# Kernel tuning notes

Measured on AMD Instinct MI355X. Metric: run time of the kernel, lower is better.

Reference implementation:

```python
import jax, jax.numpy as jnp
import numpy as np

B, S, D = 2, 2048, 2048
H, HKV, HD = 16, 4, 128
GROUPS = H // HKV
SCALE = HD ** -0.5
ROPE_THETA = 10000.0
NEG = -1e9


def _rope_cos_sin():
    inv_freq = 1.0 / (ROPE_THETA ** (jnp.arange(0, HD, 2, dtype=jnp.float32) / HD))  # [HD/2]
    pos = jnp.arange(S, dtype=jnp.float32)
    freqs = pos[:, None] * inv_freq[None, :]            # [S, HD/2]
    emb = jnp.concatenate([freqs, freqs], axis=-1)      # [S, HD]
    cos = jnp.broadcast_to(jnp.cos(emb)[None], (B, S, HD))
    sin = jnp.broadcast_to(jnp.sin(emb)[None], (B, S, HD))
    return cos, sin


def setup_inputs() -> dict:
    key = jax.random.key(0)
    ks = jax.random.split(key, 5)
    hidden_states = jax.random.normal(ks[0], (B, S, D), dtype=jnp.float32)
    cos, sin = _rope_cos_sin()
    causal = jnp.where(jnp.arange(S)[:, None] >= jnp.arange(S)[None, :], 0.0, NEG).astype(jnp.float32)
    attn_mask = jnp.broadcast_to(causal[None, None], (B, 1, S, S))
    wq = jax.random.normal(ks[1], (H * HD, D), dtype=jnp.float32) * (D ** -0.5)
    wk = jax.random.normal(ks[2], (HKV * HD, D), dtype=jnp.float32) * (D ** -0.5)
    wv = jax.random.normal(ks[3], (HKV * HD, D), dtype=jnp.float32) * (D ** -0.5)
    wo = jax.random.normal(ks[4], (D, H * HD), dtype=jnp.float32) * (D ** -0.5)
    return {"hidden_states": hidden_states, "cos": cos, "sin": sin,
            "attn_mask": attn_mask, "wq": wq, "wk": wk, "wv": wv, "wo": wo}


def _rotate_half(x):
    x1, x2 = x[..., : HD // 2], x[..., HD // 2:]
    return jnp.concatenate([-x2, x1], axis=-1)


def reference(hidden_states, cos, sin, attn_mask, wq, wk, wv, wo):
    # projections (torch Linear: x @ W.T), reshape to [B, heads, S, HD]
    q = (hidden_states @ wq.T).reshape(B, S, H, HD).transpose(0, 2, 1, 3)
    k = (hidden_states @ wk.T).reshape(B, S, HKV, HD).transpose(0, 2, 1, 3)
    v = (hidden_states @ wv.T).reshape(B, S, HKV, HD).transpose(0, 2, 1, 3)
    # RoPE (cos/sin broadcast over head dim)
    c = cos[:, None, :, :]
    s = sin[:, None, :, :]
    q = q * c + _rotate_half(q) * s
    k = k * c + _rotate_half(k) * s
    # GQA: repeat each kv head GROUPS times consecutively (matches repeat_kv)
    k = jnp.repeat(k, GROUPS, axis=1)
    v = jnp.repeat(v, GROUPS, axis=1)
    logits = jnp.einsum('bhqd,bhkd->bhqk', q, k) * SCALE + attn_mask
    w = jax.nn.softmax(logits.astype(jnp.float32), axis=-1).astype(q.dtype)
    out = jnp.einsum('bhqk,bhkd->bhqd', w, v)            # [B,H,S,HD]
    out = out.transpose(0, 2, 1, 3).reshape(B, S, H * HD)
    return out @ wo.T
```

## Files before the change

kernel.cpp:

```cpp
#include <hip/hip_runtime.h>

typedef __attribute__((ext_vector_type(8))) short bf16x8;
typedef __attribute__((ext_vector_type(4))) float f32x4;
typedef __attribute__((ext_vector_type(8))) unsigned short u16x8;
typedef unsigned short u16;

#define GLOBAL_AS __attribute__((address_space(1)))
#define LDS_AS __attribute__((address_space(3)))

#define S_ 2048
#define SCALE_ 0.08838834764831845f

static __device__ __forceinline__ u16 f2bf(float f) {
  unsigned u = __builtin_bit_cast(unsigned, f);
  u += 0x7fffu + ((u >> 16) & 1u);
  return (u16)(u >> 16);
}
static __device__ __forceinline__ float bf2f(u16 h) {
  return __builtin_bit_cast(float, ((unsigned)h) << 16);
}

__global__ __launch_bounds__(256) void cvt_bf16(const float* __restrict__ src,
                                                u16* __restrict__ dst, long n) {
  long i = ((long)blockIdx.x * 256 + threadIdx.x) * 8;
  if (i >= n) return;
  f32x4 a = *(const f32x4*)(src + i);
  f32x4 b = *(const f32x4*)(src + i + 4);
  u16x8 o;
  o[0] = f2bf(a[0]); o[1] = f2bf(a[1]); o[2] = f2bf(a[2]); o[3] = f2bf(a[3]);
  o[4] = f2bf(b[0]); o[5] = f2bf(b[1]); o[6] = f2bf(b[2]); o[7] = f2bf(b[3]);
  *(u16x8*)(dst + i) = o;
}

template <bool BF16OUT>
__global__ __launch_bounds__(256)
void gemm_bt(const u16* __restrict__ A, const u16* __restrict__ Bw,
             void* __restrict__ Cp, int M, int N, int K) {
  __shared__ u16 As[128 * 64];
  __shared__ u16 Bs[128 * 64];
  const int tid = threadIdx.x;
  const int wave = tid >> 6, lane = tid & 63;
  const int fr = lane & 15, fg = lane >> 4;
  const int wm = (wave >> 1) * 64, wn = (wave & 1) * 64;
  const long rowA = (long)blockIdx.y * 128;
  const long rowB = (long)blockIdx.x * 128;

  f32x4 acc[4][4] = {};

  for (int k0 = 0; k0 < K; k0 += 64) {
    __syncthreads();
#pragma unroll
    for (int c = 0; c < 4; ++c) {
      const int base = (wave * 4 + c) * 1024;
      const int off = base + lane * 16;
      const int r = off >> 7;
      const int kc = (off & 127) >> 1;
      __builtin_amdgcn_global_load_lds(
          (GLOBAL_AS void*)(A + (rowA + r) * (long)K + k0 + kc),
          (LDS_AS void*)(As + (base >> 1)), 16, 0, 0);
      __builtin_amdgcn_global_load_lds(
          (GLOBAL_AS void*)(Bw + (rowB + r) * (long)K + k0 + kc),
          (LDS_AS void*)(Bs + (base >> 1)), 16, 0, 0);
    }
    __syncthreads();
#pragma unroll
    for (int ks = 0; ks < 2; ++ks) {
      bf16x8 af[4], bfr[4];
#pragma unroll
      for (int i = 0; i < 4; ++i) {
        af[i]  = *(const bf16x8*)&As[(wm + i * 16 + fr) * 64 + ks * 32 + fg * 8];
        bfr[i] = *(const bf16x8*)&Bs[(wn + i * 16 + fr) * 64 + ks * 32 + fg * 8];
      }
#pragma unroll
      for (int i = 0; i < 4; ++i)
#pragma unroll
        for (int j = 0; j < 4; ++j)
          acc[i][j] = __builtin_amdgcn_mfma_f32_16x16x32_bf16(af[i], bfr[j], acc[i][j], 0, 0, 0);
    }
  }
#pragma unroll
  for (int i = 0; i < 4; ++i)
#pragma unroll
    for (int j = 0; j < 4; ++j)
#pragma unroll
      for (int r = 0; r < 4; ++r) {
        const long row = rowA + wm + i * 16 + fg * 4 + r;
        const long col = rowB + wn + j * 16 + fr;
        if (BF16OUT) ((u16*)Cp)[row * N + col] = f2bf(acc[i][j][r]);
        else         ((float*)Cp)[row * N + col] = acc[i][j][r];
      }
}

__global__ __launch_bounds__(256)
void rope_rearrange(const u16* __restrict__ QKV, const float* __restrict__ cosb,
                    const float* __restrict__ sinb, u16* __restrict__ Qr,
                    u16* __restrict__ Kr) {
  const int m = blockIdx.x;
  const int b = m >> 11, s = m & 2047;
  const int t = threadIdx.x;
  const u16* row = QKV + (long)m * 3072;
  const float* cp = cosb + (long)m * 128;
  const float* sp = sinb + (long)m * 128;
#pragma unroll
  for (int i = 0; i < 4; ++i) {
    const int idx = i * 256 + t;
    const int h = idx >> 6, d = idx & 63;
    const float x1 = bf2f(row[h * 128 + d]);
    const float x2 = bf2f(row[h * 128 + d + 64]);
    const float c = cp[d], sv = sp[d];
    const long o = ((long)(b * 16 + h) * S_ + s) * 128 + d;
    Qr[o] = f2bf(x1 * c - x2 * sv);
    Qr[o + 64] = f2bf(x2 * c + x1 * sv);
  }
  {
    const int h = t >> 6, d = t & 63;
    const float x1 = bf2f(row[2048 + h * 128 + d]);
    const float x2 = bf2f(row[2048 + h * 128 + d + 64]);
    const float c = cp[d], sv = sp[d];
    const long o = ((long)(b * 4 + h) * S_ + s) * 128 + d;
    Kr[o] = f2bf(x1 * c - x2 * sv);
    Kr[o + 64] = f2bf(x2 * c + x1 * sv);
  }
}

__global__ __launch_bounds__(256)
void transpose_v(const u16* __restrict__ QKV, u16* __restrict__ Vt) {
  __shared__ u16 t[32][33];
  const int s0 = blockIdx.x * 32, d0 = blockIdx.y * 32;
  const int bk = blockIdx.z;
  const int b = bk >> 2, kh = bk & 3;
  const int tx = threadIdx.x & 31, ty = threadIdx.x >> 5;
  const u16* src = QKV + 2560 + (long)kh * 128;
#pragma unroll
  for (int i = 0; i < 4; ++i) {
    const int sl = ty + i * 8;
    t[sl][tx] = src[(long)(b * S_ + s0 + sl) * 3072 + d0 + tx];
  }
  __syncthreads();
  u16* dst = Vt + (long)(b * 4 + kh) * 128 * S_;
#pragma unroll
  for (int i = 0; i < 4; ++i) {
    const int dl = ty + i * 8;
    dst[(long)(d0 + dl) * S_ + s0 + tx] = t[tx][dl];
  }
}

#define KVBLK 64
__global__ __launch_bounds__(256)
void attn_fwd(const u16* __restrict__ Qr, const u16* __restrict__ Kr,
              const u16* __restrict__ Vt, u16* __restrict__ Att) {
  __shared__ u16 Ks[KVBLK * 128];
  __shared__ u16 Vs[128 * KVBLK];
  __shared__ u16 Ps[4][16 * KVBLK];

  const int bh = blockIdx.y;
  const int b = bh >> 4, h = bh & 15;
  const int kh = h >> 2;
  const int tid = threadIdx.x, wave = tid >> 6, lane = tid & 63;
  const int fr = lane & 15, fg = lane >> 4;
  const int f7 = fr & 7;

  const u16* Qb = Qr + (long)(b * 16 + h) * S_ * 128;
  const u16* Kb = Kr + (long)(b * 4 + kh) * S_ * 128;
  const u16* Vg = Vt + (long)(b * 4 + kh) * 128 * (long)S_;
  u16* Pw = Ps[wave];

  for (int half = 0; half < 2; ++half) {
    const int qt = half ? (31 - blockIdx.x) : blockIdx.x;
    const int q0 = qt * 64;
    const int qbase = q0 + wave * 16;

    bf16x8 qf[4];
#pragma unroll
    for (int ks = 0; ks < 4; ++ks)
      qf[ks] = *(const bf16x8*)&Qb[(long)(qbase + fr) * 128 + ks * 32 + fg * 8];

    f32x4 acc[8] = {};
    float m_run[4], l_run[4];
#pragma unroll
    for (int r = 0; r < 4; ++r) { m_run[r] = -1e30f; l_run[r] = 0.f; }

    const int ntiles = qt + 1;
    for (int t = 0; t < ntiles; ++t) {
      const int kv0 = t * KVBLK;
      __syncthreads();
#pragma unroll
      for (int c = 0; c < 4; ++c) {
        const int slab = wave * 4 + c;
        const int offu = slab * 512 + lane * 8;
        const int kvl = offu >> 7;
        const int kc = ((offu >> 3) & 15) ^ (kvl & 7);
        __builtin_amdgcn_global_load_lds(
            (GLOBAL_AS void*)(Kb + (long)(kv0 + kvl) * 128 + kc * 8),
            (LDS_AS void*)(Ks + slab * 512), 16, 0, 0);
        const int dr = offu >> 6;
        const int vc = ((offu >> 3) & 7) ^ (dr & 7);
        __builtin_amdgcn_global_load_lds(
            (GLOBAL_AS void*)(Vg + (long)dr * S_ + kv0 + vc * 8),
            (LDS_AS void*)(Vs + slab * 512), 16, 0, 0);
      }
      __syncthreads();

      f32x4 sf[4] = {};
#pragma unroll
      for (int ks = 0; ks < 4; ++ks) {
        bf16x8 kf[4];
#pragma unroll
        for (int ni = 0; ni < 4; ++ni)
          kf[ni] = *(const bf16x8*)&Ks[(ni * 16 + fr) * 128 + (((ks * 4 + fg) ^ f7) << 3)];
        __builtin_amdgcn_s_setprio(1);
#pragma unroll
        for (int ni = 0; ni < 4; ++ni)
          sf[ni] = __builtin_amdgcn_mfma_f32_16x16x32_bf16(qf[ks], kf[ni], sf[ni], 0, 0, 0);
        __builtin_amdgcn_s_setprio(0);
      }

      float pr[4][4];
      float mx[4];
#pragma unroll
      for (int r = 0; r < 4; ++r) mx[r] = -3.0e38f;
#pragma unroll
      for (int ni = 0; ni < 4; ++ni) {
        const int kvg = kv0 + ni * 16 + fr;
#pragma unroll
        for (int r = 0; r < 4; ++r) {
          const int qrow = qbase + fg * 4 + r;
          float v = sf[ni][r] * SCALE_;
          if (kvg > qrow) v = -1e30f;
          pr[ni][r] = v;
          mx[r] = fmaxf(mx[r], v);
        }
      }
#pragma unroll
      for (int r = 0; r < 4; ++r) {
        mx[r] = fmaxf(mx[r], __shfl_xor(mx[r], 1));
        mx[r] = fmaxf(mx[r], __shfl_xor(mx[r], 2));
        mx[r] = fmaxf(mx[r], __shfl_xor(mx[r], 4));
        mx[r] = fmaxf(mx[r], __shfl_xor(mx[r], 8));
      }
      bool need = false;
#pragma unroll
      for (int r = 0; r < 4; ++r) need = need || (mx[r] > m_run[r] + 8.0f);
      if (__any(need)) {
#pragma unroll
        for (int r = 0; r < 4; ++r) {
          const float mn = fmaxf(m_run[r], mx[r]);
          const float scq = __expf(m_run[r] - mn);
          l_run[r] *= scq;
          m_run[r] = mn;
#pragma unroll
          for (int nj = 0; nj < 8; ++nj) acc[nj][r] *= scq;
        }
      }
      float rs[4] = {0.f, 0.f, 0.f, 0.f};
#pragma unroll
      for (int ni = 0; ni < 4; ++ni) {
        const int col = ni * 16 + fr;
        const int chs = col >> 3, wi = col & 7;
#pragma unroll
        for (int r = 0; r < 4; ++r) {
          const float e = __expf(pr[ni][r] - m_run[r]);
          rs[r] += e;
          const int row = fg * 4 + r;
          Pw[row * 64 + (((chs ^ (row & 7)) << 3) | wi)] = f2bf(e);
        }
      }
#pragma unroll
      for (int r = 0; r < 4; ++r) {
        rs[r] += __shfl_xor(rs[r], 1);
        rs[r] += __shfl_xor(rs[r], 2);
        rs[r] += __shfl_xor(rs[r], 4);
        rs[r] += __shfl_xor(rs[r], 8);
        l_run[r] += rs[r];
      }

      bf16x8 pf[2];
#pragma unroll
      for (int ks2 = 0; ks2 < 2; ++ks2)
        pf[ks2] = *(const bf16x8*)&Pw[fr * 64 + (((ks2 * 4 + fg) ^ f7) << 3)];
      __builtin_amdgcn_s_setprio(1);
#pragma unroll
      for (int nj = 0; nj < 8; ++nj) {
#pragma unroll
        for (int ks2 = 0; ks2 < 2; ++ks2) {
          const bf16x8 vf = *(const bf16x8*)&Vs[(nj * 16 + fr) * 64 + (((ks2 * 4 + fg) ^ f7) << 3)];
          acc[nj] = __builtin_amdgcn_mfma_f32_16x16x32_bf16(pf[ks2], vf, acc[nj], 0, 0, 0);
        }
      }
      __builtin_amdgcn_s_setprio(0);
    }

#pragma unroll
    for (int r = 0; r < 4; ++r) {
      const float inv = 1.0f / l_run[r];
      const long orow = ((long)b * S_ + qbase + fg * 4 + r) * 2048 + h * 128;
#pragma unroll
      for (int nj = 0; nj < 8; ++nj)
        Att[orow + nj * 16 + fr] = f2bf(acc[nj][r] * inv);
    }
  }
}

extern "C" void kernel_launch(void* const* d_in, const int* in_sizes, int n_in,
                              void* d_out, int out_size, void* d_ws, size_t ws_size,
                              hipStream_t stream) {
  const float* hidden = (const float*)d_in[0];
  const float* cosb = (const float*)d_in[1];
  const float* sinb = (const float*)d_in[2];
  const float* wq = (const float*)d_in[4];
  const float* wk = (const float*)d_in[5];
  const float* wv = (const float*)d_in[6];
  const float* wo = (const float*)d_in[7];
  float* out = (float*)d_out;

  u16* Xbf  = (u16*)d_ws;
  u16* Wqkv = Xbf + 8388608;
  u16* Wo   = Wqkv + 6291456;
  u16* QKV  = Wo + 4194304;
  u16* Qr   = QKV + 12582912;
  u16* Kr   = Qr + 8388608;
  u16* Vtp  = Kr + 2097152;
  u16* Att  = Xbf;
  if (ws_size < (size_t)44040192 * 2) return;

  cvt_bf16<<<dim3(4096), dim3(256), 0, stream>>>(hidden, Xbf, (long)8388608);
  cvt_bf16<<<dim3(2048), dim3(256), 0, stream>>>(wq, Wqkv, (long)4194304);
  cvt_bf16<<<dim3(512),  dim3(256), 0, stream>>>(wk, Wqkv + 4194304, (long)1048576);
  cvt_bf16<<<dim3(512),  dim3(256), 0, stream>>>(wv, Wqkv + 5242880, (long)1048576);
  cvt_bf16<<<dim3(2048), dim3(256), 0, stream>>>(wo, Wo, (long)4194304);

  gemm_bt<true><<<dim3(24, 32), dim3(256), 0, stream>>>(Xbf, Wqkv, (void*)QKV, 4096, 3072, 2048);
  rope_rearrange<<<dim3(4096), dim3(256), 0, stream>>>(QKV, cosb, sinb, Qr, Kr);
  transpose_v<<<dim3(64, 4, 8), dim3(256), 0, stream>>>(QKV, Vtp);
  attn_fwd<<<dim3(16, 32), dim3(256), 0, stream>>>(Qr, Kr, Vtp, Att);
  gemm_bt<false><<<dim3(16, 32), dim3(256), 0, stream>>>(Att, Wo, (void*)out, 4096, 2048, 2048);
}
```

Before: 268.0 us.

## Rewrite attention with 32x32 MFMA, register-resident P, and merged conversion launch

The attention kernel moves to 32x32x16 MFMAs with 128-row query tiles, computing S transposed so P stays in registers (packed via cvt_pk_bf16 and permlane32_swap) instead of going through LDS. Softmax scale and log2(e) are folded into K during RoPE so raw v_exp_f32 can be used. The five conversion launches are merged into one kernel. Trade-offs: more registers per lane, and causal imbalance because each block handles a single q tile with no pairing; waves whose rows are fully masked still take part in the loads and only skip compute.

```diff
diff --git a/kernel.cpp b/kernel.cpp
--- a/kernel.cpp
+++ b/kernel.cpp
@@ -2,7 +2,9 @@
 
 typedef __attribute__((ext_vector_type(8))) short bf16x8;
 typedef __attribute__((ext_vector_type(4))) float f32x4;
+typedef __attribute__((ext_vector_type(16))) float f32x16;
 typedef __attribute__((ext_vector_type(8))) unsigned short u16x8;
+typedef __attribute__((ext_vector_type(4))) unsigned u32x4;
 typedef unsigned short u16;
 
 #define GLOBAL_AS __attribute__((address_space(1)))
@@ -10,6 +12,7 @@
 
 #define S_ 2048
 #define SCALE_ 0.08838834764831845f
+#define SMK_ 0.12751741406106783f
 
 static __device__ __forceinline__ u16 f2bf(float f) {
   unsigned u = __builtin_bit_cast(unsigned, f);
@@ -19,11 +22,26 @@
 static __device__ __forceinline__ float bf2f(u16 h) {
   return __builtin_bit_cast(float, ((unsigned)h) << 16);
 }
-
-__global__ __launch_bounds__(256) void cvt_bf16(const float* __restrict__ src,
-                                                u16* __restrict__ dst, long n) {
-  long i = ((long)blockIdx.x * 256 + threadIdx.x) * 8;
-  if (i >= n) return;
+static __device__ __forceinline__ float exp2_raw(float x) {
+  float r; asm("v_exp_f32 %0, %1" : "=v"(r) : "v"(x)); return r;
+}
+static __device__ __forceinline__ unsigned cvtpk(float lo, float hi_) {
+  unsigned r; asm("v_cvt_pk_bf16_f32 %0, %1, %2" : "=v"(r) : "v"(lo), "v"(hi_)); return r;
+}
+
+__global__ __launch_bounds__(256)
+void cvt_all(const float* __restrict__ h, const float* __restrict__ wq,
+             const float* __restrict__ wk, const float* __restrict__ wv,
+             const float* __restrict__ wo, u16* __restrict__ Xbf,
+             u16* __restrict__ Wqkv, u16* __restrict__ Wo) {
+  const int bid = blockIdx.x;
+  const float* src; u16* dst; long base;
+  if (bid < 4096)      { src = h;  dst = Xbf;            base = (long)bid * 2048; }
+  else if (bid < 6144) { src = wq; dst = Wqkv;           base = (long)(bid - 4096) * 2048; }
+  else if (bid < 6656) { src = wk; dst = Wqkv + 4194304; base = (long)(bid - 6144) * 2048; }
+  else if (bid < 7168) { src = wv; dst = Wqkv + 5242880; base = (long)(bid - 6656) * 2048; }
+  else                 { src = wo; dst = Wo;             base = (long)(bid - 7168) * 2048; }
+  const long i = base + (long)threadIdx.x * 8;
   f32x4 a = *(const f32x4*)(src + i);
   f32x4 b = *(const f32x4*)(src + i + 4);
   u16x8 o;
@@ -118,8 +136,8 @@
     const float x2 = bf2f(row[2048 + h * 128 + d + 64]);
     const float c = cp[d], sv = sp[d];
     const long o = ((long)(b * 4 + h) * S_ + s) * 128 + d;
-    Kr[o] = f2bf(x1 * c - x2 * sv);
-    Kr[o + 64] = f2bf(x2 * c + x1 * sv);
+    Kr[o] = f2bf((x1 * c - x2 * sv) * SMK_);
+    Kr[o + 64] = f2bf((x2 * c + x1 * sv) * SMK_);
   }
 }
 
@@ -145,159 +163,151 @@
   }
 }
 
-#define KVBLK 64
+struct PA2 { bf16x8 a, b; };
+static __device__ __forceinline__ PA2 pack_half(const f32x16 s) {
+  PA2 out;
+#pragma unroll
+  for (int ks2 = 0; ks2 < 2; ++ks2) {
+    const int rb = ks2 * 8;
+    unsigned w0 = cvtpk(s[rb + 0], s[rb + 1]);
+    unsigned w1 = cvtpk(s[rb + 2], s[rb + 3]);
+    unsigned w2 = cvtpk(s[rb + 4], s[rb + 5]);
+    unsigned w3 = cvtpk(s[rb + 6], s[rb + 7]);
+    asm("v_permlane32_swap_b32 %0, %1" : "+v"(w0), "+v"(w2));
+    asm("v_permlane32_swap_b32 %0, %1" : "+v"(w1), "+v"(w3));
+    u32x4 pw; pw[0] = w0; pw[1] = w1; pw[2] = w2; pw[3] = w3;
+    if (ks2 == 0) out.a = __builtin_bit_cast(bf16x8, pw);
+    else          out.b = __builtin_bit_cast(bf16x8, pw);
+  }
+  return out;
+}
+
 __global__ __launch_bounds__(256)
 void attn_fwd(const u16* __restrict__ Qr, const u16* __restrict__ Kr,
               const u16* __restrict__ Vt, u16* __restrict__ Att) {
-  __shared__ u16 Ks[KVBLK * 128];
-  __shared__ u16 Vs[128 * KVBLK];
-  __shared__ u16 Ps[4][16 * KVBLK];
+  __shared__ u16 Ks[64 * 128];
+  __shared__ u16 Vs[128 * 64];
 
   const int bh = blockIdx.y;
   const int b = bh >> 4, h = bh & 15;
   const int kh = h >> 2;
+  const int qt = 15 - blockIdx.x;
+  const int q0 = qt * 128;
   const int tid = threadIdx.x, wave = tid >> 6, lane = tid & 63;
-  const int fr = lane & 15, fg = lane >> 4;
-  const int f7 = fr & 7;
+  const int l31 = lane & 31, hi = lane >> 5, r7 = lane & 7;
+  const int qwmin = q0 + wave * 32;
 
   const u16* Qb = Qr + (long)(b * 16 + h) * S_ * 128;
   const u16* Kb = Kr + (long)(b * 4 + kh) * S_ * 128;
   const u16* Vg = Vt + (long)(b * 4 + kh) * 128 * (long)S_;
-  u16* Pw = Ps[wave];
-
-  for (int half = 0; half < 2; ++half) {
-    const int qt = half ? (31 - blockIdx.x) : blockIdx.x;
-    const int q0 = qt * 64;
-    const int qbase = q0 + wave * 16;
-
-    bf16x8 qf[4];
-#pragma unroll
-    for (int ks = 0; ks < 4; ++ks)
-      qf[ks] = *(const bf16x8*)&Qb[(long)(qbase + fr) * 128 + ks * 32 + fg * 8];
-
-    f32x4 acc[8] = {};
-    float m_run[4], l_run[4];
-#pragma unroll
-    for (int r = 0; r < 4; ++r) { m_run[r] = -1e30f; l_run[r] = 0.f; }
-
-    const int ntiles = qt + 1;
-    for (int t = 0; t < ntiles; ++t) {
-      const int kv0 = t * KVBLK;
-      __syncthreads();
-#pragma unroll
-      for (int c = 0; c < 4; ++c) {
-        const int slab = wave * 4 + c;
-        const int offu = slab * 512 + lane * 8;
-        const int kvl = offu >> 7;
-        const int kc = ((offu >> 3) & 15) ^ (kvl & 7);
-        __builtin_amdgcn_global_load_lds(
-            (GLOBAL_AS void*)(Kb + (long)(kv0 + kvl) * 128 + kc * 8),
-            (LDS_AS void*)(Ks + slab * 512), 16, 0, 0);
-        const int dr = offu >> 6;
-        const int vc = ((offu >> 3) & 7) ^ (dr & 7);
-        __builtin_amdgcn_global_load_lds(
-            (GLOBAL_AS void*)(Vg + (long)dr * S_ + kv0 + vc * 8),
-            (LDS_AS void*)(Vs + slab * 512), 16, 0, 0);
-      }
-      __syncthreads();
-
-      f32x4 sf[4] = {};
+
+  bf16x8 qf[8];
+  const u16* qrow = Qb + (long)(qwmin + l31) * 128 + hi * 8;
+#pragma unroll
+  for (int ds = 0; ds < 8; ++ds) qf[ds] = *(const bf16x8*)(qrow + ds * 16);
+
+  f32x16 acc[4] = {};
+  float m_run = -1e30f, l_run = 0.f;
+  const int qg = qwmin + l31;
+
+  const int ntiles = 2 * (qt + 1);
+  for (int t = 0; t < ntiles; ++t) {
+    const int kv0 = t * 64;
+    __syncthreads();
+#pragma unroll
+    for (int c = 0; c < 4; ++c) {
+      const int slab = wave * 4 + c;
+      const int offu = slab * 512 + lane * 8;
+      const int kvl = offu >> 7;
+      const int kc = ((offu >> 3) & 15) ^ (kvl & 7);
+      __builtin_amdgcn_global_load_lds(
+          (GLOBAL_AS void*)(Kb + (long)(kv0 + kvl) * 128 + kc * 8),
+          (LDS_AS void*)(Ks + slab * 512), 16, 0, 0);
+      const int dr = offu >> 6;
+      const int vc = ((offu >> 3) & 7) ^ (dr & 7);
+      __builtin_amdgcn_global_load_lds(
+          (GLOBAL_AS void*)(Vg + (long)dr * S_ + kv0 + vc * 8),
+          (LDS_AS void*)(Vs + slab * 512), 16, 0, 0);
+    }
+    __syncthreads();
+
+    if (kv0 > qwmin + 31) continue;
+
+    f32x16 s0 = {}, s1 = {};
+    __builtin_amdgcn_s_setprio(1);
+#pragma unroll
+    for (int ds = 0; ds < 8; ++ds) {
+      const int ch = ((2 * ds + hi) ^ r7) << 3;
+      const bf16x8 ka0 = *(const bf16x8*)&Ks[l31 * 128 + ch];
+      const bf16x8 ka1 = *(const bf16x8*)&Ks[(32 + l31) * 128 + ch];
+      s0 = __builtin_amdgcn_mfma_f32_32x32x16_bf16(ka0, qf[ds], s0, 0, 0, 0);
+      s1 = __builtin_amdgcn_mfma_f32_32x32x16_bf16(ka1, qf[ds], s1, 0, 0, 0);
+    }
+    __builtin_amdgcn_s_setprio(0);
+
+    if (kv0 + 63 > qwmin) {
+#pragma unroll
+      for (int r = 0; r < 16; ++r) {
+        const int cr = (r & 3) + 8 * (r >> 2) + 4 * hi;
+        if (kv0 + cr > qg)      s0[r] = -3.0e38f;
+        if (kv0 + 32 + cr > qg) s1[r] = -3.0e38f;
+      }
+    }
+
+    float mx = s0[0];
+#pragma unroll
+    for (int r = 1; r < 16; ++r) mx = fmaxf(mx, s0[r]);
+#pragma unroll
+    for (int r = 0; r < 16; ++r) mx = fmaxf(mx, s1[r]);
+    mx = fmaxf(mx, __shfl_xor(mx, 32));
+
+    if (__any(mx > m_run + 8.0f)) {
+      const float mn = fmaxf(m_run, mx);
+      const float scq = exp2_raw(m_run - mn);
+      m_run = mn; l_run *= scq;
+#pragma unroll
+      for (int r = 0; r < 16; ++r) {
+        const int cr = (r & 3) + 8 * (r >> 2) + 4 * hi;
+        const float sr = __shfl(scq, cr);
+        acc[0][r] *= sr; acc[1][r] *= sr; acc[2][r] *= sr; acc[3][r] *= sr;
+      }
+    }
+
+    float rs = 0.f;
+#pragma unroll
+    for (int r = 0; r < 16; ++r) { s0[r] = exp2_raw(s0[r] - m_run); rs += s0[r]; }
+#pragma unroll
+    for (int r = 0; r < 16; ++r) { s1[r] = exp2_raw(s1[r] - m_run); rs += s1[r]; }
+    rs += __shfl_xor(rs, 32);
+    l_run += rs;
+
+    bf16x8 pa[4];
+    { PA2 p0 = pack_half(s0); pa[0] = p0.a; pa[1] = p0.b; }
+    { PA2 p1 = pack_half(s1); pa[2] = p1.a; pa[3] = p1.b; }
+
+    __builtin_amdgcn_s_setprio(1);
+#pragma unroll
+    for (int nj = 0; nj < 4; ++nj) {
+      const int vrow = (nj * 32 + l31) * 64;
 #pragma unroll
       for (int ks = 0; ks < 4; ++ks) {
-        bf16x8 kf[4];
-#pragma unroll
-        for (int ni = 0; ni < 4; ++ni)
-          kf[ni] = *(const bf16x8*)&Ks[(ni * 16 + fr) * 128 + (((ks * 4 + fg) ^ f7) << 3)];
-        __builtin_amdgcn_s_setprio(1);
-#pragma unroll
-        for (int ni = 0; ni < 4; ++ni)
-          sf[ni] = __builtin_amdgcn_mfma_f32_16x16x32_bf16(qf[ks], kf[ni], sf[ni], 0, 0, 0);
-        __builtin_amdgcn_s_setprio(0);
-      }
-
-      float pr[4][4];
-      float mx[4];
-#pragma unroll
-      for (int r = 0; r < 4; ++r) mx[r] = -3.0e38f;
-#pragma unroll
-      for (int ni = 0; ni < 4; ++ni) {
-        const int kvg = kv0 + ni * 16 + fr;
-#pragma unroll
-        for (int r = 0; r < 4; ++r) {
-          const int qrow = qbase + fg * 4 + r;
-          float v = sf[ni][r] * SCALE_;
-          if (kvg > qrow) v = -1e30f;
-          pr[ni][r] = v;
-          mx[r] = fmaxf(mx[r], v);
-        }
-      }
-#pragma unroll
-      for (int r = 0; r < 4; ++r) {
-        mx[r] = fmaxf(mx[r], __shfl_xor(mx[r], 1));
-        mx[r] = fmaxf(mx[r], __shfl_xor(mx[r], 2));
-        mx[r] = fmaxf(mx[r], __shfl_xor(mx[r], 4));
-        mx[r] = fmaxf(mx[r], __shfl_xor(mx[r], 8));
-      }
-      bool need = false;
-#pragma unroll
-      for (int r = 0; r < 4; ++r) need = need || (mx[r] > m_run[r] + 8.0f);
-      if (__any(need)) {
-#pragma unroll
-        for (int r = 0; r < 4; ++r) {
-          const float mn = fmaxf(m_run[r], mx[r]);
-          const float scq = __expf(m_run[r] - mn);
-          l_run[r] *= scq;
-          m_run[r] = mn;
-#pragma unroll
-          for (int nj = 0; nj < 8; ++nj) acc[nj][r] *= scq;
-        }
-      }
-      float rs[4] = {0.f, 0.f, 0.f, 0.f};
-#pragma unroll
-      for (int ni = 0; ni < 4; ++ni) {
-        const int col = ni * 16 + fr;
-        const int chs = col >> 3, wi = col & 7;
-#pragma unroll
-        for (int r = 0; r < 4; ++r) {
-          const float e = __expf(pr[ni][r] - m_run[r]);
-          rs[r] += e;
-          const int row = fg * 4 + r;
-          Pw[row * 64 + (((chs ^ (row & 7)) << 3) | wi)] = f2bf(e);
-        }
-      }
-#pragma unroll
-      for (int r = 0; r < 4; ++r) {
-        rs[r] += __shfl_xor(rs[r], 1);
-        rs[r] += __shfl_xor(rs[r], 2);
-        rs[r] += __shfl_xor(rs[r], 4);
-        rs[r] += __shfl_xor(rs[r], 8);
-        l_run[r] += rs[r];
-      }
-
-      bf16x8 pf[2];
-#pragma unroll
-      for (int ks2 = 0; ks2 < 2; ++ks2)
-        pf[ks2] = *(const bf16x8*)&Pw[fr * 64 + (((ks2 * 4 + fg) ^ f7) << 3)];
-      __builtin_amdgcn_s_setprio(1);
-#pragma unroll
-      for (int nj = 0; nj < 8; ++nj) {
-#pragma unroll
-        for (int ks2 = 0; ks2 < 2; ++ks2) {
-          const bf16x8 vf = *(const bf16x8*)&Vs[(nj * 16 + fr) * 64 + (((ks2 * 4 + fg) ^ f7) << 3)];
-          acc[nj] = __builtin_amdgcn_mfma_f32_16x16x32_bf16(pf[ks2], vf, acc[nj], 0, 0, 0);
-        }
-      }
-      __builtin_amdgcn_s_setprio(0);
-    }
-
-#pragma unroll
-    for (int r = 0; r < 4; ++r) {
-      const float inv = 1.0f / l_run[r];
-      const long orow = ((long)b * S_ + qbase + fg * 4 + r) * 2048 + h * 128;
-#pragma unroll
-      for (int nj = 0; nj < 8; ++nj)
-        Att[orow + nj * 16 + fr] = f2bf(acc[nj][r] * inv);
-    }
+        const bf16x8 vf = *(const bf16x8*)&Vs[vrow + (((2 * ks + hi) ^ r7) << 3)];
+        acc[nj] = __builtin_amdgcn_mfma_f32_32x32x16_bf16(pa[ks], vf, acc[nj], 0, 0, 0);
+      }
+    }
+    __builtin_amdgcn_s_setprio(0);
+  }
+
+  const float inv = 1.0f / l_run;
+#pragma unroll
+  for (int r = 0; r < 16; ++r) {
+    const int cr = (r & 3) + 8 * (r >> 2) + 4 * hi;
+    const float ir = __shfl(inv, cr);
+    const long orow = ((long)b * S_ + q0 + wave * 32 + cr) * 2048 + h * 128 + l31;
+    Att[orow]      = f2bf(acc[0][r] * ir);
+    Att[orow + 32] = f2bf(acc[1][r] * ir);
+    Att[orow + 64] = f2bf(acc[2][r] * ir);
+    Att[orow + 96] = f2bf(acc[3][r] * ir);
   }
 }
 
@@ -323,12 +333,7 @@
   u16* Att  = Xbf;
   if (ws_size < (size_t)44040192 * 2) return;
 
-  cvt_bf16<<<dim3(4096), dim3(256), 0, stream>>>(hidden, Xbf, (long)8388608);
-  cvt_bf16<<<dim3(2048), dim3(256), 0, stream>>>(wq, Wqkv, (long)4194304);
-  cvt_bf16<<<dim3(512),  dim3(256), 0, stream>>>(wk, Wqkv + 4194304, (long)1048576);
-  cvt_bf16<<<dim3(512),  dim3(256), 0, stream>>>(wv, Wqkv + 5242880, (long)1048576);
-  cvt_bf16<<<dim3(2048), dim3(256), 0, stream>>>(wo, Wo, (long)4194304);
-
+  cvt_all<<<dim3(9216), dim3(256), 0, stream>>>(hidden, wq, wk, wv, wo, Xbf, Wqkv, Wo);
   gemm_bt<true><<<dim3(24, 32), dim3(256), 0, stream>>>(Xbf, Wqkv, (void*)QKV, 4096, 3072, 2048);
   rope_rearrange<<<dim3(4096), dim3(256), 0, stream>>>(QKV, cosb, sinb, Qr, Kr);
   transpose_v<<<dim3(64, 4, 8), dim3(256), 0, stream>>>(QKV, Vtp);
```

New measurement: 295.4 us. 10.2% more time.
